# Kernel tuning notes

Hardware: AMD Instinct MI355X
Metric: run time of the kernel (lower is better)

The kernel has to match this reference:

```python
import jax, jax.numpy as jnp
import numpy as np
import math

B, C, H, W = 8, 64, 128, 128
OUT, HEADS, K, S = 32, 8, 3, 2
DH = C // HEADS
PAD = (K - 1) // 2
EPS = 1e-5


def _unfold(t, k):
    # t: [B, C, H, W] -> per-pixel kxk windows [B*H*W, k*k, C] (torch.nn.Unfold layout: channel-major)
    b, c, h, w = t.shape
    pat = jax.lax.conv_general_dilated_patches(t, (k, k), (1, 1), [(PAD, PAD), (PAD, PAD)])  # [B, C*k*k, H, W]
    pat = pat.reshape(b, c, k * k, h * w)          # [B, C, k^2, HW]
    return jnp.transpose(pat, (0, 3, 2, 1)).reshape(b * h * w, k * k, c)


def setup_inputs() -> dict:
    key = jax.random.key(0)
    ks = jax.random.split(key, 18)
    def n(k, shape, sc=0.05):
        return jax.random.normal(k, shape, jnp.float32) * sc
    return {
        "x": jax.random.normal(ks[0], (B, C, H, W), jnp.float32),
        "up_query": jax.random.normal(ks[1], (1, S * S, C), jnp.float32),  # learned up-sampling queries
        "Wk": n(ks[2], (C, C)), "bk": n(ks[3], (C,), 0.02),   # to_k 1x1 conv
        "Wv": n(ks[4], (C, C)), "bv": n(ks[5], (C,), 0.02),   # to_v 1x1 conv
        "Wq": n(ks[6], (C, C)), "bq": n(ks[7], (C,), 0.02),   # MHA q proj
        "Wka": n(ks[8], (C, C)), "bka": n(ks[9], (C,), 0.02), # MHA k proj
        "Wva": n(ks[10], (C, C)), "bva": n(ks[11], (C,), 0.02),  # MHA v proj
        "Wo": n(ks[12], (C, OUT)), "bo": n(ks[13], (OUT,), 0.02),  # MHA output proj (project_dim=out_dim)
        "rel_pos": n(ks[14], (1, HEADS, S * S, K * K), 1.0),  # learned relative positional bias
        "ln_g": jnp.ones((OUT,), jnp.float32),
        "ln_b": jnp.zeros((OUT,), jnp.float32),
    }


def reference(x, up_query, Wk, bk, Wv, bv, Wq, bq, Wka, bka, Wva, bva, Wo, bo, rel_pos, ln_g, ln_b):
    b, c, h, w = x.shape
    # pre_norm = Identity (post_norm=True). pe_k = Identity (pos_embedding=None).
    kf = jnp.einsum('bchw,cd->bdhw', x, Wk) + bk[None, :, None, None]
    vf = jnp.einsum('bchw,cd->bdhw', x, Wv) + bv[None, :, None, None]
    # aux_zeros branch: to_k(pe(zeros)) == conv bias -> adds bk to every window position
    xk = _unfold(kf, K) + bk[None, None, :]            # [N, k^2, C]
    xv = _unfold(vf, K)                                # [N, k^2, C]
    n = xk.shape[0]
    xq = jnp.broadcast_to(up_query, (n, S * S, c))     # [N, s^2, C]
    # multi-head attention with relative positional bias on logits
    qh = (xq @ Wq + bq).reshape(n, S * S, HEADS, DH)
    kh = (xk @ Wka + bka).reshape(n, K * K, HEADS, DH)
    vh = (xv @ Wva + bva).reshape(n, K * K, HEADS, DH)
    logits = jnp.einsum('nqhd,nkhd->nhqk', qh, kh) / math.sqrt(DH) + rel_pos  # [N, h, s^2, k^2]
    attn = jax.nn.softmax(logits, axis=-1)
    out = jnp.einsum('nhqk,nkhd->nqhd', attn, vh).reshape(n, S * S, c)
    out = out @ Wo + bo                                # [N, s^2, OUT]
    # post LayerNorm over out_dim
    mu = jnp.mean(out, axis=-1, keepdims=True)
    var = jnp.mean(jnp.square(out - mu), axis=-1, keepdims=True)
    out = (out - mu) / jnp.sqrt(var + EPS) * ln_g + ln_b
    # pixel-shuffle style reshape to [B, OUT, H*s, W*s]
    out = out.reshape(b, h, w, S, S, OUT)
    out = jnp.transpose(out, (0, 5, 1, 3, 2, 4)).reshape(b, OUT, h * S, w * S)
    return out
```

## Files before the change

### kernel.cpp

```cpp
#include <hip/hip_runtime.h>

#define HW    16384
#define WIDTH 128
#define LOG2E    1.4426950408889634f
#define RS_LOG2E 0.5101464200926166f

#define WFB_DWORDS 4992
#define WOT_OFF    4992
#define REL_OFF    6016
#define WS_DWORDS  6304

typedef short bshort8 __attribute__((ext_vector_type(8)));
typedef _Float16 half8 __attribute__((ext_vector_type(8)));
typedef float f32x4   __attribute__((ext_vector_type(4)));
typedef unsigned u32x4 __attribute__((ext_vector_type(4)));
typedef unsigned u32x2 __attribute__((ext_vector_type(2)));

static __device__ inline unsigned short f2bf(float f) {
    unsigned u = __builtin_bit_cast(unsigned, f);
    unsigned r = u + 0x7fff + ((u >> 16) & 1);
    return (unsigned short)(r >> 16);
}
static __device__ inline unsigned cvtpk(float lo, float hi) {
    unsigned d;
    asm("v_cvt_pk_bf16_f32 %0, %1, %2" : "=v"(d) : "v"(lo), "v"(hi));
    return d;
}
static __device__ inline unsigned pkrtz(float lo, float hi) {
    return __builtin_bit_cast(unsigned, __builtin_amdgcn_cvt_pkrtz(lo, hi));
}
static __device__ inline float lo16f(unsigned u) {
    return (float)__builtin_bit_cast(_Float16, (unsigned short)(u & 0xffffu));
}
static __device__ inline float hi16f(unsigned u) {
    return (float)__builtin_bit_cast(_Float16, (unsigned short)(u >> 16));
}
static __device__ inline unsigned pkfma16_lo(unsigned o, unsigned a, unsigned v) {
    asm("v_pk_fma_f16 %0, %1, %2, %0 op_sel:[0,0,0] op_sel_hi:[0,1,1]"
        : "+v"(o) : "v"(a), "v"(v));
    return o;
}
static __device__ inline unsigned pkfma16_hi(unsigned o, unsigned a, unsigned v) {
    asm("v_pk_fma_f16 %0, %1, %2, %0 op_sel:[1,0,0] op_sel_hi:[1,1,1]"
        : "+v"(o) : "v"(a), "v"(v));
    return o;
}
static __device__ inline unsigned pkmul16_lo(unsigned a, unsigned r) {
    unsigned d;
    asm("v_pk_mul_f16 %0, %1, %2 op_sel:[0,0] op_sel_hi:[0,1]"
        : "=v"(d) : "v"(r), "v"(a));
    return d;
}
static __device__ inline unsigned pkmul16_hi(unsigned a, unsigned r) {
    unsigned d;
    asm("v_pk_mul_f16 %0, %1, %2 op_sel:[1,0] op_sel_hi:[1,1]"
        : "=v"(d) : "v"(r), "v"(a));
    return d;
}

__global__ __launch_bounds__(256) void k0_fuse(
    const float* __restrict__ up_query,
    const float* __restrict__ Wk, const float* __restrict__ bk,
    const float* __restrict__ Wv, const float* __restrict__ bv,
    const float* __restrict__ Wq, const float* __restrict__ bq,
    const float* __restrict__ Wka, const float* __restrict__ bka,
    const float* __restrict__ Wva, const float* __restrict__ bva,
    const float* __restrict__ Wo, const float* __restrict__ rel_pos,
    float* __restrict__ ws)
{
    __shared__ float qcS[4][64];
    __shared__ float WkT[64][65];
    __shared__ float WvT[64][65];
    __shared__ float colS[12][64];
    __shared__ float bred[12][8];
    __shared__ float pred[12][8];

    const int tid = threadIdx.x;
    const int bj  = blockIdx.x;
    const int j0  = bj * 12;

    {
        int q = tid >> 6, f = tid & 63;
        float a = bq[f];
        for (int c = 0; c < 64; ++c) a = fmaf(up_query[q*64+c], Wq[c*64+f], a);
        qcS[q][f] = a;
    }
    for (int i = tid; i < 4096; i += 256) {
        int c = i >> 6, e = i & 63;
        WkT[e][c] = Wk[i];
        WvT[e][c] = Wv[i];
    }
    __syncthreads();

    for (int i = tid; i < 768; i += 256) {
        int jl = i >> 6, e = i & 63;
        int j = j0 + jl;
        float v;
        if (j < 32) {
            int h = j >> 2, qq = j & 3;
            float s = 0.f;
            #pragma unroll
            for (int d = 0; d < 8; ++d)
                s = fmaf(Wka[e*64 + h*8 + d], qcS[qq][h*8 + d], s);
            v = s * RS_LOG2E;
        } else {
            v = Wva[e*64 + (j - 32)];
        }
        colS[jl][e] = v;
    }
    if (tid < 96) {
        int jl = tid >> 3, d = tid & 7;
        int j = j0 + jl;
        if (j < 32) {
            int h = j >> 2, qq = j & 3;
            int fi = h*8 + d;
            float bW = 0.f;
            for (int e = 0; e < 64; ++e) bW = fmaf(bk[e], Wka[e*64 + fi], bW);
            float qv = qcS[qq][fi];
            bred[jl][d] = (2.f*bW + bka[fi]) * qv;
            pred[jl][d] = bW * qv;
        } else {
            float s = 0.f;
            for (int e = d*8; e < d*8 + 8; ++e)
                s = fmaf(bv[e], Wva[e*64 + (j - 32)], s);
            bred[jl][d] = s;
            pred[jl][d] = 0.f;
        }
    }
    __syncthreads();

    unsigned* wsd = (unsigned*)ws;
    for (int i = tid; i < 384; i += 256) {
        int cp = i & 31, jl = i >> 5;
        int j = j0 + jl;
        const float (*MT)[65] = (j < 32) ? WkT : WvT;
        float o0 = 0.f, o1 = 0.f;
        for (int e = 0; e < 64; ++e) {
            float cv = colS[jl][e];
            o0 = fmaf(MT[e][2*cp],     cv, o0);
            o1 = fmaf(MT[e][2*cp + 1], cv, o1);
        }
        wsd[j*52 + cp] = (unsigned)f2bf(o0) | ((unsigned)f2bf(o1) << 16);
    }
    for (int i = tid; i < 240; i += 256) {
        int jl = i / 20, kd = 32 + (i % 20);
        int j = j0 + jl;
        unsigned val = 0u;
        if (kd == 32) {
            float sv = 0.f, sp = 0.f;
            #pragma unroll
            for (int d = 0; d < 8; ++d) { sv += bred[jl][d]; sp += pred[jl][d]; }
            float bf_, pd_;
            if (j < 32) { bf_ = sv * RS_LOG2E; pd_ = (sv - sp) * RS_LOG2E; }
            else        { bf_ = sv + bva[j-32]; pd_ = bva[j-32]; }
            val = (unsigned)f2bf(bf_) | ((unsigned)f2bf(pd_) << 16);
        }
        wsd[j*52 + kd] = val;
    }
    if (bj == 7) {
        for (int i = tid; i < 1024; i += 256) {
            int col = i >> 5, kp = i & 31;
            wsd[WOT_OFF + i] = pkrtz(Wo[(2*kp)*32 + col], Wo[(2*kp + 1)*32 + col]);
        }
        for (int i = tid; i < 288; i += 256)
            ws[REL_OFF + i] = rel_pos[i] * LOG2E;
    }
}

__global__ __launch_bounds__(256, 5) void k2_attn(
    const float* __restrict__ x, const float* __restrict__ ws,
    const float* __restrict__ bo,
    const float* __restrict__ ln_g, const float* __restrict__ ln_b,
    float* __restrict__ out)
{
    __shared__ __align__(16) char smem[32768];

    const int tid = threadIdx.x;

    const int flat = blockIdx.x;
    const int wg   = (flat & 7) * 256 + (flat >> 3);
    const int tx = wg & 15;
    const int ty = (wg >> 4) & 15;
    const int b  = wg >> 8;

    #pragma unroll
    for (int it = 0; it < 5; ++it) {
        int i = tid + it*256;
        if (i < 1200) {
            int kq = (int)(((unsigned)i * 5243u) >> 19);
            int p  = i - kq*100;
            int py = p / 10, px = p - py*10;
            int gy = ty*8 - 1 + py, gx = tx*8 - 1 + px;
            bool valid = ((unsigned)gy < 128u) && ((unsigned)gx < 128u);
            u32x4 pack = {0u, 0u, 0u, 0u};
            if (kq < 8) {
                if (valid) {
                    const float* xp = x + ((size_t)b*64 + kq*8)*HW + gy*WIDTH + gx;
                    #pragma unroll
                    for (int e = 0; e < 4; ++e)
                        pack[e] = cvtpk(xp[(size_t)(2*e)*HW], xp[(size_t)(2*e+1)*HW]);
                }
            } else if (kq == 8) {
                pack[0] = valid ? 0x00003f80u : 0x3f800000u;
            }
            *(u32x4*)(smem + kq*1792 + p*16) = pack;
        }
    }
    __syncthreads();

    const int lane = tid & 63;
    const int wv   = tid >> 6;
    const int frow = lane & 15;
    const int kseg = lane >> 4;

    const unsigned short* wfs = (const unsigned short*)ws;
    f32x4 accs[12];
    #pragma unroll
    for (int mi = 0; mi < 2; ++mi) {
        const int mt = wv*2 + mi;
        if (mt < 7) {
            const int prow = mt*16 + frow;
            bshort8 xa0 = *(const bshort8*)(smem + (0*4 + kseg)*1792 + prow*16);
            bshort8 xa1 = *(const bshort8*)(smem + (1*4 + kseg)*1792 + prow*16);
            bshort8 xa2 = *(const bshort8*)(smem + (2*4 + kseg)*1792 + prow*16);
            #pragma unroll
            for (int nt = 0; nt < 6; ++nt) {
                const unsigned short* wrow = wfs + (nt*16 + frow)*104 + kseg*8;
                f32x4 acc = {0.f, 0.f, 0.f, 0.f};
                acc = __builtin_amdgcn_mfma_f32_16x16x32_bf16(*(const bshort8*)(wrow),      xa0, acc, 0, 0, 0);
                acc = __builtin_amdgcn_mfma_f32_16x16x32_bf16(*(const bshort8*)(wrow + 32), xa1, acc, 0, 0, 0);
                acc = __builtin_amdgcn_mfma_f32_16x16x32_bf16(*(const bshort8*)(wrow + 64), xa2, acc, 0, 0, 0);
                accs[mi*6 + nt] = acc;
            }
        }
    }
    __syncthreads();

    unsigned short* Lh = (unsigned short*)smem;
    char*           Vb = smem + 8192;
    #pragma unroll
    for (int mi = 0; mi < 2; ++mi) {
        const int mt = wv*2 + mi;
        if (mt < 7) {
            const int p = mt*16 + frow;
            if (p < 100) {
                const unsigned vsw = (((unsigned)(p >> 3)) & 7u) << 4;
                #pragma unroll
                for (int nt = 0; nt < 6; ++nt) {
                    const f32x4 acc = accs[mi*6 + nt];
                    u32x2 dd = { pkrtz(acc[0], acc[1]), pkrtz(acc[2], acc[3]) };
                    if (nt < 2) {
                        *(u32x2*)(Lh + p*36 + nt*16 + kseg*4) = dd;
                    } else {
                        unsigned off = ((unsigned)((nt-2)*32 + kseg*8)) ^ vsw;
                        *(u32x2*)(Vb + p*144 + off) = dd;
                    }
                }
            }
        }
    }
    __syncthreads();

    const int dpy = lane >> 3, dpx = lane & 7;
    const int pbase = dpy*10 + dpx;
    const float* relw = ws + REL_OFF;

    unsigned od[32];
    #pragma unroll
    for (int hh = 0; hh < 2; ++hh) {
        const int h = wv*2 + hh;
        unsigned apk[2][9];
        float s0 = 0.f, s1 = 0.f, s2 = 0.f, s3 = 0.f;
        const float* rp = relw + h*36;
        #pragma unroll
        for (int n = 0; n < 9; ++n) {
            const int off = (n/3)*10 + (n%3);
            const u32x2 L4 = *(const u32x2*)(Lh + (pbase + off)*36 + h*4);
            float e0 = exp2f(lo16f(L4[0]) + rp[n]);
            float e1 = exp2f(hi16f(L4[0]) + rp[9 + n]);
            float e2 = exp2f(lo16f(L4[1]) + rp[18 + n]);
            float e3 = exp2f(hi16f(L4[1]) + rp[27 + n]);
            s0 += e0; s1 += e1; s2 += e2; s3 += e3;
            apk[0][n] = pkrtz(e0, e1);
            apk[1][n] = pkrtz(e2, e3);
        }
        const unsigned r01 = pkrtz(__builtin_amdgcn_rcpf(s0), __builtin_amdgcn_rcpf(s1));
        const unsigned r23 = pkrtz(__builtin_amdgcn_rcpf(s2), __builtin_amdgcn_rcpf(s3));

        unsigned o16[4][4] = {{0u,0u,0u,0u},{0u,0u,0u,0u},{0u,0u,0u,0u},{0u,0u,0u,0u}};
        #pragma unroll
        for (int n = 0; n < 9; ++n) {
            const int pp = pbase + (n/3)*10 + (n%3);
            const unsigned voff = ((unsigned)(h*16)) ^ ((((unsigned)(pp >> 3)) & 7u) << 4);
            const u32x4 v4 = *(const u32x4*)(Vb + pp*144 + voff);
            #pragma unroll
            for (int j = 0; j < 4; ++j) {
                o16[0][j] = pkfma16_lo(o16[0][j], apk[0][n], v4[j]);
                o16[1][j] = pkfma16_hi(o16[1][j], apk[0][n], v4[j]);
                o16[2][j] = pkfma16_lo(o16[2][j], apk[1][n], v4[j]);
                o16[3][j] = pkfma16_hi(o16[3][j], apk[1][n], v4[j]);
            }
        }
        #pragma unroll
        for (int j = 0; j < 4; ++j) {
            od[(0*2 + hh)*4 + j] = pkmul16_lo(o16[0][j], r01);
            od[(1*2 + hh)*4 + j] = pkmul16_hi(o16[1][j], r01);
            od[(2*2 + hh)*4 + j] = pkmul16_lo(o16[2][j], r23);
            od[(3*2 + hh)*4 + j] = pkmul16_hi(o16[3][j], r23);
        }
    }
    __syncthreads();

    {
        const unsigned sw = ((unsigned)(lane & 7)) << 4;
        #pragma unroll
        for (int q = 0; q < 4; ++q) {
            const int row = lane*4 + q;
            #pragma unroll
            for (int hh = 0; hh < 2; ++hh) {
                u32x4 w4 = { od[(q*2+hh)*4+0], od[(q*2+hh)*4+1],
                             od[(q*2+hh)*4+2], od[(q*2+hh)*4+3] };
                *(u32x4*)(smem + row*128 + (((unsigned)(wv*32 + hh*16)) ^ sw)) = w4;
            }
        }
    }
    __syncthreads();

    const unsigned short* wotu = (const unsigned short*)ws + WOT_OFF*2;
    half8 av[4][2];
    #pragma unroll
    for (int mt = 0; mt < 4; ++mt) {
        const int row = wv*64 + mt*16 + frow;
        const unsigned sw = (((unsigned)(row >> 2)) & 7u) << 4;
        #pragma unroll
        for (int ks = 0; ks < 2; ++ks)
            av[mt][ks] = __builtin_bit_cast(half8,
                *(const u32x4*)(smem + row*128 + (((unsigned)(kseg*16 + ks*64)) ^ sw)));
    }
    half8 bv_[2][2];
    #pragma unroll
    for (int nt = 0; nt < 2; ++nt) {
        const int col = nt*16 + frow;
        #pragma unroll
        for (int ks = 0; ks < 2; ++ks)
            bv_[nt][ks] = __builtin_bit_cast(half8,
                *(const u32x4*)(wotu + col*64 + kseg*8 + ks*32));
    }
    f32x4 cacc[4][2];
    #pragma unroll
    for (int mt = 0; mt < 4; ++mt)
        #pragma unroll
        for (int nt = 0; nt < 2; ++nt)
            cacc[mt][nt] = (f32x4){0.f, 0.f, 0.f, 0.f};
    #pragma unroll
    for (int ks = 0; ks < 2; ++ks)
        #pragma unroll
        for (int mt = 0; mt < 4; ++mt)
            #pragma unroll
            for (int nt = 0; nt < 2; ++nt)
                cacc[mt][nt] = __builtin_amdgcn_mfma_f32_16x16x32_f16(
                    av[mt][ks], bv_[nt][ks], cacc[mt][nt], 0, 0, 0);

    #pragma unroll
    for (int mt = 0; mt < 4; ++mt)
        #pragma unroll
        for (int nt = 0; nt < 2; ++nt)
            #pragma unroll
            for (int r = 0; r < 4; ++r) {
                const int row = wv*64 + mt*16 + kseg*4 + r;
                const int col = nt*16 + frow;
                *(float*)(smem + row*128
                    + (((unsigned)(col*4)) ^ ((((unsigned)(row >> 2)) & 7u) << 4)))
                    = cacc[mt][nt][r];
            }
    asm volatile("s_waitcnt lgkmcnt(0)" ::: "memory");

    float cv[32];
    {
        const unsigned sw = (((unsigned)(tid >> 2)) & 7u) << 4;
        #pragma unroll
        for (int j = 0; j < 8; ++j) {
            const f32x4 c4 = *(const f32x4*)(smem + tid*128 + (((unsigned)(j*16)) ^ sw));
            cv[j*4+0] = c4[0]; cv[j*4+1] = c4[1]; cv[j*4+2] = c4[2]; cv[j*4+3] = c4[3];
        }
    }
    float mu = 0.f;
    #pragma unroll
    for (int oc = 0; oc < 32; ++oc) { cv[oc] += bo[oc]; mu += cv[oc]; }
    mu *= (1.f/32.f);
    float var = 0.f;
    #pragma unroll
    for (int oc = 0; oc < 32; ++oc) { float d = cv[oc] - mu; var += d*d; }
    var *= (1.f/32.f);
    const float rstd = rsqrtf(var + 1e-5f);

    const int q   = tid & 3;
    const int pix = tid >> 2;
    const int gy = ty*8 + (pix >> 3), gx = tx*8 + (pix & 7);
    const int Y = gy*2 + (q >> 1), X = gx*2 + (q & 1);
    float* op = out + (((size_t)b*32)*256 + Y)*256 + X;
    #pragma unroll
    for (int oc = 0; oc < 32; ++oc) {
        float v = (cv[oc] - mu) * rstd * ln_g[oc] + ln_b[oc];
        op[(size_t)oc * 65536] = v;
    }
}

extern "C" void kernel_launch(void* const* d_in, const int* in_sizes, int n_in,
                              void* d_out, int out_size, void* d_ws, size_t ws_size,
                              hipStream_t stream)
{
    const float* x        = (const float*)d_in[0];
    const float* up_query = (const float*)d_in[1];
    const float* Wk  = (const float*)d_in[2];
    const float* bk  = (const float*)d_in[3];
    const float* Wv  = (const float*)d_in[4];
    const float* bv  = (const float*)d_in[5];
    const float* Wq  = (const float*)d_in[6];
    const float* bq  = (const float*)d_in[7];
    const float* Wka = (const float*)d_in[8];
    const float* bka = (const float*)d_in[9];
    const float* Wva = (const float*)d_in[10];
    const float* bva = (const float*)d_in[11];
    const float* Wo  = (const float*)d_in[12];
    const float* bo  = (const float*)d_in[13];
    const float* rel_pos = (const float*)d_in[14];
    const float* ln_g = (const float*)d_in[15];
    const float* ln_b = (const float*)d_in[16];

    float* ws  = (float*)d_ws;
    float* out = (float*)d_out;

    if (ws_size < (size_t)WS_DWORDS * 4) return;

    k0_fuse<<<8, 256, 0, stream>>>(up_query, Wk, bk, Wv, bv, Wq, bq,
                                   Wka, bka, Wva, bva, Wo, rel_pos, ws);
    k2_attn<<<2048, 256, 0, stream>>>(x, ws, bo, ln_g, ln_b, out);
}
```

Measured before the change: 63.71 us.

## Load halo pixel pairs with float2, drop V swizzle, add setprio around compute

The halo staging loop now handles two adjacent pixels per thread, using float2 global loads when both are in bounds, which halves the iteration count and widens the memory accesses. The XOR swizzle on the V tile in shared memory is removed so addresses become simple base-plus-offset. s_setprio is raised around the MFMA and packed-FMA sections so compute wavefronts get issue priority. Removing the swizzle may bring back LDS bank conflicts, and float2 loads at odd x offsets are only 8-byte aligned when gx0 is even.

```diff
diff --git a/kernel.cpp b/kernel.cpp
--- a/kernel.cpp
+++ b/kernel.cpp
@@ -184,26 +184,45 @@
     const int b  = wg >> 8;
 
     #pragma unroll
-    for (int it = 0; it < 5; ++it) {
+    for (int it = 0; it < 3; ++it) {
         int i = tid + it*256;
-        if (i < 1200) {
-            int kq = (int)(((unsigned)i * 5243u) >> 19);
-            int p  = i - kq*100;
-            int py = p / 10, px = p - py*10;
-            int gy = ty*8 - 1 + py, gx = tx*8 - 1 + px;
-            bool valid = ((unsigned)gy < 128u) && ((unsigned)gx < 128u);
-            u32x4 pack = {0u, 0u, 0u, 0u};
+        if (i < 600) {
+            int kq = i / 50;
+            int pp = i - kq*50;
+            int p0 = pp*2;
+            int py = p0/10; int px0 = p0 - py*10;
+            int gy = ty*8 - 1 + py, gx0 = tx*8 - 1 + px0;
+            bool vy = (unsigned)gy < 128u;
+            bool v0 = vy && ((unsigned)gx0 < 128u);
+            bool v1 = vy && ((unsigned)(gx0+1) < 128u);
+            u32x4 pk0 = {0u,0u,0u,0u}, pk1 = {0u,0u,0u,0u};
             if (kq < 8) {
-                if (valid) {
-                    const float* xp = x + ((size_t)b*64 + kq*8)*HW + gy*WIDTH + gx;
+                const float* xp = x + ((size_t)b*64 + kq*8)*HW + gy*WIDTH + gx0;
+                if (v0 && v1) {
                     #pragma unroll
-                    for (int e = 0; e < 4; ++e)
-                        pack[e] = cvtpk(xp[(size_t)(2*e)*HW], xp[(size_t)(2*e+1)*HW]);
+                    for (int e = 0; e < 4; ++e) {
+                        float2 c0 = *(const float2*)(xp + (size_t)(2*e)*HW);
+                        float2 c1 = *(const float2*)(xp + (size_t)(2*e+1)*HW);
+                        pk0[e] = cvtpk(c0.x, c1.x);
+                        pk1[e] = cvtpk(c0.y, c1.y);
+                    }
+                } else if (v0 || v1) {
+                    #pragma unroll
+                    for (int e = 0; e < 4; ++e) {
+                        float a0 = 0.f, b0 = 0.f, a1 = 0.f, b1 = 0.f;
+                        if (v0) { a0 = xp[(size_t)(2*e)*HW];     b0 = xp[(size_t)(2*e+1)*HW]; }
+                        if (v1) { a1 = xp[(size_t)(2*e)*HW + 1]; b1 = xp[(size_t)(2*e+1)*HW + 1]; }
+                        pk0[e] = cvtpk(a0, b0);
+                        pk1[e] = cvtpk(a1, b1);
+                    }
                 }
             } else if (kq == 8) {
-                pack[0] = valid ? 0x00003f80u : 0x3f800000u;
-            }
-            *(u32x4*)(smem + kq*1792 + p*16) = pack;
+                pk0[0] = v0 ? 0x00003f80u : 0x3f800000u;
+                pk1[0] = v1 ? 0x00003f80u : 0x3f800000u;
+            }
+            char* dst = smem + kq*1792 + p0*16;
+            *(u32x4*)(dst)      = pk0;
+            *(u32x4*)(dst + 16) = pk1;
         }
     }
     __syncthreads();
@@ -215,6 +234,7 @@
 
     const unsigned short* wfs = (const unsigned short*)ws;
     f32x4 accs[12];
+    __builtin_amdgcn_s_setprio(1);
     #pragma unroll
     for (int mi = 0; mi < 2; ++mi) {
         const int mt = wv*2 + mi;
@@ -234,6 +254,7 @@
             }
         }
     }
+    __builtin_amdgcn_s_setprio(0);
     __syncthreads();
 
     unsigned short* Lh = (unsigned short*)smem;
@@ -244,7 +265,6 @@
         if (mt < 7) {
             const int p = mt*16 + frow;
             if (p < 100) {
-                const unsigned vsw = (((unsigned)(p >> 3)) & 7u) << 4;
                 #pragma unroll
                 for (int nt = 0; nt < 6; ++nt) {
                     const f32x4 acc = accs[mi*6 + nt];
@@ -252,8 +272,7 @@
                     if (nt < 2) {
                         *(u32x2*)(Lh + p*36 + nt*16 + kseg*4) = dd;
                     } else {
-                        unsigned off = ((unsigned)((nt-2)*32 + kseg*8)) ^ vsw;
-                        *(u32x2*)(Vb + p*144 + off) = dd;
+                        *(u32x2*)(Vb + p*144 + (nt-2)*32 + kseg*8) = dd;
                     }
                 }
             }
@@ -272,10 +291,11 @@
         unsigned apk[2][9];
         float s0 = 0.f, s1 = 0.f, s2 = 0.f, s3 = 0.f;
         const float* rp = relw + h*36;
+        const unsigned short* lbase = Lh + pbase*36 + h*4;
         #pragma unroll
         for (int n = 0; n < 9; ++n) {
             const int off = (n/3)*10 + (n%3);
-            const u32x2 L4 = *(const u32x2*)(Lh + (pbase + off)*36 + h*4);
+            const u32x2 L4 = *(const u32x2*)(lbase + off*36);
             float e0 = exp2f(lo16f(L4[0]) + rp[n]);
             float e1 = exp2f(hi16f(L4[0]) + rp[9 + n]);
             float e2 = exp2f(lo16f(L4[1]) + rp[18 + n]);
@@ -288,11 +308,12 @@
         const unsigned r23 = pkrtz(__builtin_amdgcn_rcpf(s2), __builtin_amdgcn_rcpf(s3));
 
         unsigned o16[4][4] = {{0u,0u,0u,0u},{0u,0u,0u,0u},{0u,0u,0u,0u},{0u,0u,0u,0u}};
+        const char* vbase = Vb + pbase*144 + h*16;
+        __builtin_amdgcn_s_setprio(1);
         #pragma unroll
         for (int n = 0; n < 9; ++n) {
-            const int pp = pbase + (n/3)*10 + (n%3);
-            const unsigned voff = ((unsigned)(h*16)) ^ ((((unsigned)(pp >> 3)) & 7u) << 4);
-            const u32x4 v4 = *(const u32x4*)(Vb + pp*144 + voff);
+            const int off = (n/3)*10 + (n%3);
+            const u32x4 v4 = *(const u32x4*)(vbase + off*144);
             #pragma unroll
             for (int j = 0; j < 4; ++j) {
                 o16[0][j] = pkfma16_lo(o16[0][j], apk[0][n], v4[j]);
@@ -301,6 +322,7 @@
                 o16[3][j] = pkfma16_hi(o16[3][j], apk[1][n], v4[j]);
             }
         }
+        __builtin_amdgcn_s_setprio(0);
         #pragma unroll
         for (int j = 0; j < 4; ++j) {
             od[(0*2 + hh)*4 + j] = pkmul16_lo(o16[0][j], r01);
@@ -352,6 +374,7 @@
         #pragma unroll
         for (int nt = 0; nt < 2; ++nt)
             cacc[mt][nt] = (f32x4){0.f, 0.f, 0.f, 0.f};
+    __builtin_amdgcn_s_setprio(1);
     #pragma unroll
     for (int ks = 0; ks < 2; ++ks)
         #pragma unroll
@@ -360,6 +383,7 @@
             for (int nt = 0; nt < 2; ++nt)
                 cacc[mt][nt] = __builtin_amdgcn_mfma_f32_16x16x32_f16(
                     av[mt][ks], bv_[nt][ks], cacc[mt][nt], 0, 0, 0);
+    __builtin_amdgcn_s_setprio(0);
 
     #pragma unroll
     for (int mt = 0; mt < 4; ++mt)
```

New measurement: 65.05 us. 1.02x slower.
